# Kernel tuning notes

Measured on AMD Instinct MI355X. Metric: run time of the kernel, lower is better.

The kernel has to match this reference:

```python
import jax, jax.numpy as jnp
import numpy as np

B, M, N, P, H = 8192, 4, 2, 2, 128
D5 = M * 5            # FC5 output = m * in_mult_KNet
D2H = (H + H) * 40    # FC2 hidden = d_input_FC2 * out_mult_KNet


def _lin(x, W, b):
    return x @ W.T + b


def _gru(x, h, Wih, Whh, bih, bhh):
    # PyTorch GRU cell math (single layer, single step)
    gi = x @ Wih.T + bih   # [B, 3H]
    gh = h @ Whh.T + bhh   # [B, 3H]
    ir, iz, inn = jnp.split(gi, 3, axis=-1)
    hr, hz, hn = jnp.split(gh, 3, axis=-1)
    r = jax.nn.sigmoid(ir + hr)
    z = jax.nn.sigmoid(iz + hz)
    n = jnp.tanh(inn + r * hn)
    return (1.0 - z) * n + z * h


def setup_inputs() -> dict:
    key = jax.random.key(0)
    ks = iter(jax.random.split(key, 64))
    rn = lambda *s: jax.random.normal(next(ks), s, dtype=jnp.float32)
    sc = lambda d: np.float32(1.0 / np.sqrt(d))
    inp = {
        'y': rn(B, N, 1), 'u': rn(B, P, 1), 'm1x_post': rn(B, M, 1),
        'h_Q': jnp.zeros((B, H), jnp.float32),
        'h_Sigma': jnp.zeros((B, H), jnp.float32),
        'h_S': jnp.zeros((B, H), jnp.float32),
        'F_mat': jnp.eye(M, dtype=jnp.float32) + 0.1 * rn(M, M),
        'G_mat': 0.1 * rn(M, P),
        'H_mat': 0.5 * rn(N, M),
        'innov_logit': jnp.float32(0.0),
        'W_fc5': rn(D5, M) * sc(M), 'b_fc5': rn(D5) * 0.01,
        'Wih_Q': rn(3 * H, D5) * sc(H), 'Whh_Q': rn(3 * H, H) * sc(H),
        'bih_Q': rn(3 * H) * 0.01, 'bhh_Q': rn(3 * H) * 0.01,
        'Wih_Sig': rn(3 * H, H) * sc(H), 'Whh_Sig': rn(3 * H, H) * sc(H),
        'bih_Sig': rn(3 * H) * 0.01, 'bhh_Sig': rn(3 * H) * 0.01,
        'W_fc1': rn(N * N, H) * sc(H), 'b_fc1': rn(N * N) * 0.01,
        'W_fc7': rn(N, N) * sc(N), 'b_fc7': rn(N) * 0.01,
        'Wih_S': rn(3 * H, N * N + N) * sc(H), 'Whh_S': rn(3 * H, H) * sc(H),
        'bih_S': rn(3 * H) * 0.01, 'bhh_S': rn(3 * H) * 0.01,
        'W_fc2a': rn(D2H, 2 * H) * sc(2 * H), 'b_fc2a': rn(D2H) * 0.01,
        'W_fc2b': rn(N * M, D2H) * sc(D2H), 'b_fc2b': rn(N * M) * 0.01,
        'W_fc3': rn(M * M, H + N * M) * sc(H + N * M), 'b_fc3': rn(M * M) * 0.01,
        'W_fc4': rn(H, H + M * M) * sc(H + M * M), 'b_fc4': rn(H) * 0.01,
    }
    return inp


def reference(y, u, m1x_post, h_Q, h_Sigma, h_S, F_mat, G_mat, H_mat, innov_logit,
              W_fc5, b_fc5, Wih_Q, Whh_Q, bih_Q, bhh_Q,
              Wih_Sig, Whh_Sig, bih_Sig, bhh_Sig,
              W_fc1, b_fc1, W_fc7, b_fc7,
              Wih_S, Whh_S, bih_S, bhh_S,
              W_fc2a, b_fc2a, W_fc2b, b_fc2b,
              W_fc3, b_fc3, W_fc4, b_fc4):
    relu = jax.nn.relu
    # --- step_prior: linear system model f(x,u)=Fx+Gu, h(x)=Hx (no normalization) ---
    x_post = m1x_post[..., 0]                      # [B, M]
    x_prior = x_post @ F_mat.T + u[..., 0] @ G_mat.T
    y_pred = x_prior @ H_mat.T                     # [B, N]
    dy = y[..., 0] - y_pred                        # innovation [B, N]
    # --- KGain_step (dropout = identity at inference) ---
    out5 = relu(_lin(x_prior, W_fc5, b_fc5))       # [B, 20]
    hQ_new = _gru(out5, h_Q, Wih_Q, Whh_Q, bih_Q, bhh_Q)
    hSig = _gru(hQ_new, h_Sigma, Wih_Sig, Whh_Sig, bih_Sig, bhh_Sig)
    out1 = relu(_lin(hSig, W_fc1, b_fc1))          # [B, n^2]
    out7 = relu(_lin(dy, W_fc7, b_fc7))            # [B, n]
    hS_new = _gru(jnp.concatenate([out1, out7], -1), h_S, Wih_S, Whh_S, bih_S, bhh_S)
    in2 = jnp.concatenate([hSig, hS_new], -1)      # [B, 256]
    out2 = _lin(relu(_lin(in2, W_fc2a, b_fc2a)), W_fc2b, b_fc2b)  # KG flat [B, n*m]
    out3 = relu(_lin(jnp.concatenate([hS_new, out2], -1), W_fc3, b_fc3))
    hSig_new = relu(_lin(jnp.concatenate([hSig, out3], -1), W_fc4, b_fc4))
    # --- posterior update ---
    KG = out2.reshape(B, M, N)
    gamma = jax.nn.sigmoid(innov_logit)
    inov = gamma * jnp.einsum('bmn,bn->bm', KG, dy)
    m1x_posterior = (x_prior + inov)[..., None]    # [B, M, 1]
    return m1x_posterior, hQ_new, hSig_new, hS_new
```

## Files before the change

kernel.cpp:

```cpp
#include <hip/hip_runtime.h>
#include <hip/hip_bf16.h>

typedef __attribute__((ext_vector_type(8))) short bf16x8;
typedef __attribute__((ext_vector_type(4))) float f32x4;
typedef __attribute__((ext_vector_type(4))) short s16x4;
typedef __attribute__((ext_vector_type(4))) float f32v4;
typedef unsigned short u16;

__device__ inline u16 f2b(float f){ __hip_bfloat16 b = __float2bfloat16(f); return __builtin_bit_cast(unsigned short, b); }
__device__ inline float b2f(u16 u){ unsigned int x = ((unsigned int)u)<<16; return __builtin_bit_cast(float, x); }
__device__ inline float sigm(float x){ return 1.f/(1.f+__expf(-x)); }
__device__ inline float tanhfast(float x){ float e = __expf(2.f*x); return 1.f - 2.f/(e+1.f); }

__device__ inline f32x4 mfma16(bf16x8 a, bf16x8 b, f32x4 c){
  return __builtin_amdgcn_mfma_f32_16x16x32_bf16(a, b, c, 0, 0, 0);
}

struct CVA {
  const float *w2a, *w2b, *wihQ, *whhQ, *wihSg, *whhSg, *wihS, *whhS, *wfc3, *wfc4;
  u16 *waB, *wbB, *wihQp, *whhQb, *wihSgB, *whhSgB, *wihSp, *whhSb, *wfc3p, *wfc4p;
};

__global__ __launch_bounds__(256) void kconv(CVA a){
  int id = blockIdx.x*256 + threadIdx.x;
  if (id < 2621440){
    int t  = id >> 12;
    int r  = id & 4095;
    int kk = r >> 9;
    int l  = (r >> 3) & 63;
    int e  = id & 7;
    int col = t*16 + (l & 15);
    int k   = kk*32 + (l >> 4)*8 + e;
    a.waB[id] = f2b(a.w2a[col*256 + k]);
    return;
  }
  id -= 2621440;
  if (id < 163840){
    int s = id >> 9;
    int r = id & 511;
    int l = r >> 3;
    int e = r & 7;
    int o = l & 15;
    int k = s*32 + (l >> 4)*8 + e;
    a.wbB[id] = (o < 8) ? f2b(a.w2b[o*10240 + k]) : (u16)0;
    return;
  }
  id -= 163840;
  if (id < 12288){ int j=id>>5, k=id&31; a.wihQp[id] = (k<20)? f2b(a.wihQ[j*20+k]) : (u16)0; return; }
  id -= 12288;
  if (id < 49152){ a.whhQb[id] = f2b(a.whhQ[id]); return; }
  id -= 49152;
  if (id < 49152){ a.wihSgB[id] = f2b(a.wihSg[id]); return; }
  id -= 49152;
  if (id < 49152){ a.whhSgB[id] = f2b(a.whhSg[id]); return; }
  id -= 49152;
  if (id < 12288){ int j=id>>5, k=id&31; a.wihSp[id] = (k<6)? f2b(a.wihS[j*6+k]) : (u16)0; return; }
  id -= 12288;
  if (id < 49152){ a.whhSb[id] = f2b(a.whhS[id]); return; }
  id -= 49152;
  if (id < 2560){ int j=id/160, k=id%160; a.wfc3p[id] = (k<136)? f2b(a.wfc3[j*136+k]) : (u16)0; return; }
  id -= 2560;
  if (id < 20480){ int j=id/160, k=id%160; a.wfc4p[id] = (k<144)? f2b(a.wfc4[j*144+k]) : (u16)0; return; }
}

template<int KX, int LDX, bool SOUT, bool GB16, bool GF32>
__device__ __forceinline__ void gru_step(
    const u16* sX, const u16* sH,
    const u16* __restrict__ Wih, const int ldwih, const u16* __restrict__ Whh,
    const float* __restrict__ bih, const float* __restrict__ bhh,
    float* __restrict__ gOutF, u16* sOut, u16* __restrict__ gB16)
{
  const int tid = threadIdx.x;
  const int w = tid>>6, lane = tid&63, c = lane&15, khi = lane>>4;
  for (int nn=0; nn<2; ++nn){
    const int n = w*2+nn;
    const int j = n*16 + c;
    const float bir=bih[j], biz=bih[128+j], bin=bih[256+j];
    const float bhr=bhh[j], bhz=bhh[128+j], bhn=bhh[256+j];
    bf16x8 BX0[KX], BX1[KX], BX2[KX], BH0[4], BH1[4], BH2[4];
    #pragma unroll
    for (int kk=0;kk<KX;++kk){
      const u16* p = Wih + j*ldwih + kk*32 + khi*8;
      BX0[kk] = *(const bf16x8*)(p);
      BX1[kk] = *(const bf16x8*)(p + 128*ldwih);
      BX2[kk] = *(const bf16x8*)(p + 256*ldwih);
    }
    #pragma unroll
    for (int kk=0;kk<4;++kk){
      const u16* p = Whh + j*128 + kk*32 + khi*8;
      BH0[kk] = *(const bf16x8*)(p);
      BH1[kk] = *(const bf16x8*)(p + 128*128);
      BH2[kk] = *(const bf16x8*)(p + 256*128);
    }
    #pragma unroll
    for (int m=0;m<2;++m){
      f32x4 ir={0,0,0,0}, iz={0,0,0,0}, inx={0,0,0,0};
      f32x4 hr={0,0,0,0}, hz={0,0,0,0}, hn={0,0,0,0};
      #pragma unroll
      for (int kk=0;kk<KX;++kk){
        bf16x8 A = *(const bf16x8*)(sX + (m*16+c)*LDX + kk*32 + khi*8);
        ir  = mfma16(A, BX0[kk], ir);
        iz  = mfma16(A, BX1[kk], iz);
        inx = mfma16(A, BX2[kk], inx);
      }
      #pragma unroll
      for (int kk=0;kk<4;++kk){
        bf16x8 A = *(const bf16x8*)(sH + (m*16+c)*136 + kk*32 + khi*8);
        hr = mfma16(A, BH0[kk], hr);
        hz = mfma16(A, BH1[kk], hz);
        hn = mfma16(A, BH2[kk], hn);
      }
      #pragma unroll
      for (int e=0;e<4;++e){
        int r = m*16 + khi*4 + e;
        float rg = sigm(ir[e]+hr[e]+bir+bhr);
        float zg = sigm(iz[e]+hz[e]+biz+bhz);
        float ng = tanhfast(inx[e]+bin + rg*(hn[e]+bhn));
        float hold = b2f(sH[r*136 + j]);
        float hv = (1.f-zg)*ng + zg*hold;
        if (GF32) gOutF[r*128 + j] = hv;
        if (SOUT) sOut[r*136 + j] = f2b(hv);
        if (GB16) gB16[r*256 + j] = f2b(hv);
      }
    }
  }
}

struct K1A {
  const float *y,*u,*m1x,*hQ,*hSg,*hS,*F,*G,*Hm,*W5,*b5,
              *bihQ,*bhhQ,*bihSg,*bhhSg,*W1,*b1,*W7,*b7,*bihS,*bhhS;
  const u16 *wihQp,*whhQ,*wihSg,*whhSg,*wihSp,*whhS;
  float *outHQ,*outHS,*xp,*dy;
  u16 *in2;
};

__device__ __forceinline__ void load_h_tile(u16* dst, const float* src, int row0){
  const int tid = threadIdx.x;
  #pragma unroll
  for (int i=0;i<4;++i){
    int f4 = tid + i*256;
    int r = f4>>5, c4 = f4&31;
    f32v4 v = *(const f32v4*)(src + (row0+r)*128 + c4*4);
    s16x4 o;
    o[0]=(short)f2b(v[0]); o[1]=(short)f2b(v[1]);
    o[2]=(short)f2b(v[2]); o[3]=(short)f2b(v[3]);
    *(s16x4*)(dst + r*136 + c4*4) = o;
  }
}

__global__ __launch_bounds__(256) void k1(K1A a){
  __shared__ u16 sX[32*40];
  __shared__ u16 sH[32*136];
  __shared__ u16 sXL[32*136];
  __shared__ u16 sSig[32*136];
  __shared__ float sDY[64];
  const int row0 = blockIdx.x*32;
  const int tid = threadIdx.x;

  load_h_tile(sH, a.hQ, row0);
  if (tid < 32){
    int r = tid, row = row0 + r;
    float xpost[4], uu[2], xpr[4];
    #pragma unroll
    for (int i=0;i<4;++i) xpost[i]=a.m1x[row*4+i];
    uu[0]=a.u[row*2]; uu[1]=a.u[row*2+1];
    #pragma unroll
    for (int i=0;i<4;++i){
      float s=0.f;
      #pragma unroll
      for (int jj=0;jj<4;++jj) s += a.F[i*4+jj]*xpost[jj];
      #pragma unroll
      for (int jj=0;jj<2;++jj) s += a.G[i*2+jj]*uu[jj];
      xpr[i]=s; a.xp[row*4+i]=s;
    }
    #pragma unroll
    for (int nn2=0;nn2<2;++nn2){
      float s=0.f;
      #pragma unroll
      for (int jj=0;jj<4;++jj) s += a.Hm[nn2*4+jj]*xpr[jj];
      float d = a.y[row*2+nn2]-s;
      a.dy[row*2+nn2]=d; sDY[r*2+nn2]=d;
    }
    #pragma unroll
    for (int o=0;o<20;++o){
      float s=a.b5[o];
      #pragma unroll
      for (int k=0;k<4;++k) s += a.W5[o*4+k]*xpr[k];
      sX[r*40+o]=f2b(fmaxf(s,0.f));
    }
    for (int o=20;o<40;++o) sX[r*40+o]=0;
  }
  __syncthreads();
  gru_step<1,40,true,false,true>(sX, sH, a.wihQp, 32, a.whhQ, a.bihQ, a.bhhQ,
                                 a.outHQ + row0*128, sXL, nullptr);
  __syncthreads();
  load_h_tile(sH, a.hSg, row0);
  __syncthreads();
  gru_step<4,136,true,true,false>(sXL, sH, a.wihSg, 128, a.whhSg, a.bihSg, a.bhhSg,
                                  nullptr, sSig, a.in2 + row0*256);
  __syncthreads();
  if (tid < 128){
    int r = tid>>2, o = tid&3;
    float s = a.b1[o];
    for (int k=0;k<128;++k) s += a.W1[o*128+k]*b2f(sSig[r*136+k]);
    sX[r*40+o] = f2b(fmaxf(s,0.f));
  } else if (tid < 192){
    int t = tid-128; int r=t>>1, o=t&1;
    float s = a.b7[o] + a.W7[o*2]*sDY[r*2] + a.W7[o*2+1]*sDY[r*2+1];
    sX[r*40+4+o] = f2b(fmaxf(s,0.f));
  }
  for (int i=tid;i<32*26;i+=256){ int r=i/26, cc=6+(i%26); sX[r*40+cc]=0; }
  load_h_tile(sH, a.hS, row0);
  __syncthreads();
  gru_step<1,40,false,true,true>(sX, sH, a.wihSp, 32, a.whhS, a.bihS, a.bhhS,
                                 a.outHS + row0*128, nullptr, a.in2 + row0*256 + 128);
}

struct K2A {
  const u16 *waB, *wbB, *in2;
  const float *b2a;
  float *parts;
};

__global__ __launch_bounds__(512) void k2(K2A a){
  __shared__ u16 sA[64*256];
  __shared__ u16 sHid[8*64*36];
  const int bid = blockIdx.x;
  const int rb = bid>>3, ch = bid&7;
  const int row0 = rb*64;
  const int tid = threadIdx.x;
  const int wid = tid>>6, lane = tid&63, c = lane&15, khi = lane>>4;

  #pragma unroll
  for (int i=0;i<8;++i){
    int idx = tid + i*512;
    int r = idx>>6, c4 = idx&63;
    s16x4 v = *(const s16x4*)(a.in2 + (size_t)(row0+r)*256 + c4*4);
    *(s16x4*)(sA + r*256 + ((c4*4) ^ ((r&7)<<3))) = v;
  }
  __syncthreads();

  u16* sHw = sHid + wid*2304;
  f32x4 C2[4];
  #pragma unroll
  for (int m=0;m<4;++m) C2[m] = (f32x4){0,0,0,0};

  for (int it=0; it<5; ++it){
    const int colb = ch*1280 + it*256 + wid*32;
    const int t0 = colb>>4;
    #pragma unroll
    for (int h=0;h<2;++h){
      bf16x8 Bf[8];
      #pragma unroll
      for (int kk=0;kk<8;++kk)
        Bf[kk] = *(const bf16x8*)(a.waB + (size_t)((t0+h)*8+kk)*512 + lane*8);
      const float bias = a.b2a[colb + h*16 + c];
      #pragma unroll
      for (int m=0;m<4;++m){
        const int row = m*16 + c;
        bf16x8 Af[8];
        #pragma unroll
        for (int kk=0;kk<8;++kk)
          Af[kk] = *(const bf16x8*)(sA + row*256 + ((kk*32 + khi*8) ^ ((row&7)<<3)));
        f32x4 c0={0,0,0,0};
        #pragma unroll
        for (int kk=0;kk<8;++kk)
          c0 = mfma16(Af[kk], Bf[kk], c0);
        #pragma unroll
        for (int e=0;e<4;++e){
          int rr = m*16 + khi*4 + e;
          sHw[rr*36 + h*16 + c] = f2b(fmaxf(c0[e]+bias, 0.f));
        }
      }
    }
    bf16x8 B2 = *(const bf16x8*)(a.wbB + (size_t)(colb>>5)*512 + lane*8);
    #pragma unroll
    for (int m=0;m<4;++m){
      bf16x8 A2 = *(const bf16x8*)(sHw + (m*16+c)*36 + khi*8);
      C2[m] = mfma16(A2, B2, C2[m]);
    }
  }
  __syncthreads();
  float* sRed = (float*)sHid;
  if (c < 8){
    #pragma unroll
    for (int m=0;m<4;++m)
      #pragma unroll
      for (int e=0;e<4;++e)
        sRed[wid*512 + (m*16+khi*4+e)*8 + c] = C2[m][e];
  }
  __syncthreads();
  {
    int i = tid;
    int r = i>>3, o = i&7;
    float s = 0.f;
    #pragma unroll
    for (int wv=0;wv<8;++wv) s += sRed[wv*512 + r*8 + o];
    a.parts[(size_t)ch*65536 + (size_t)(row0+r)*8 + o] = s;
  }
}

struct K3A {
  const float *parts;
  const float *b2b, *bfc3, *bfc4, *xp, *dy, *innov;
  const u16 *in2, *wfc3p, *wfc4p;
  float *outPost, *outHSig;
};

__global__ __launch_bounds__(256) void k3(K3A a){
  __shared__ u16 sA[64*168];
  __shared__ u16 sX4[64*168];
  __shared__ float sOut2[64*8];
  const int row0 = blockIdx.x*64;
  const int tid = threadIdx.x;
  for (int i=tid;i<512;i+=256){
    int r=i>>3, o=i&7, row=row0+r;
    float s = a.b2b[o];
    #pragma unroll
    for (int chv=0;chv<8;++chv) s += a.parts[chv*65536 + row*8 + o];
    sOut2[i]=s;
    sA[r*168+128+o]=f2b(s);
  }
  for (int i=tid;i<2048;i+=256){
    int r=i>>5, c4=i&31;
    *(s16x4*)(sA  + r*168 + c4*4) = *(const s16x4*)(a.in2 + (row0+r)*256 + 128 + c4*4);
    *(s16x4*)(sX4 + r*168 + c4*4) = *(const s16x4*)(a.in2 + (row0+r)*256 + c4*4);
  }
  for (int i=tid;i<64*6;i+=256){
    int r=i/6, c4=i%6;
    *(s16x4*)(sA + r*168 + 136 + c4*4) = (s16x4){0,0,0,0};
  }
  for (int i=tid;i<64*4;i+=256){
    int r=i>>2, c4=i&3;
    *(s16x4*)(sX4 + r*168 + 144 + c4*4) = (s16x4){0,0,0,0};
  }
  __syncthreads();
  {
    int r = tid>>2, m = tid&3, row = row0+r;
    float g = 1.f/(1.f+__expf(-a.innov[0]));
    float d0 = a.dy[row*2], d1 = a.dy[row*2+1];
    float k0 = sOut2[r*8+m*2], k1 = sOut2[r*8+m*2+1];
    a.outPost[row*4+m] = a.xp[row*4+m] + g*(k0*d0+k1*d1);
  }
  const int w = tid>>6, lane = tid&63, c = lane&15, khi = lane>>4;
  {
    f32x4 C3 = {0,0,0,0};
    #pragma unroll
    for (int kk=0;kk<5;++kk){
      bf16x8 A  = *(const bf16x8*)(sA + (w*16+c)*168 + kk*32 + khi*8);
      bf16x8 Bf = *(const bf16x8*)(a.wfc3p + c*160 + kk*32 + khi*8);
      C3 = mfma16(A,Bf,C3);
    }
    float bj = a.bfc3[c];
    #pragma unroll
    for (int e=0;e<4;++e){
      int r = w*16 + khi*4 + e;
      sX4[r*168 + 128 + c] = f2b(fmaxf(C3[e]+bj, 0.f));
    }
  }
  __syncthreads();
  for (int nn=0;nn<2;++nn){
    int j = (w*2+nn)*16 + c;
    bf16x8 Bf[5];
    #pragma unroll
    for (int kk=0;kk<5;++kk) Bf[kk] = *(const bf16x8*)(a.wfc4p + j*160 + kk*32 + khi*8);
    float bj = a.bfc4[j];
    #pragma unroll
    for (int m=0;m<4;++m){
      f32x4 C = {0,0,0,0};
      #pragma unroll
      for (int kk=0;kk<5;++kk){
        bf16x8 A = *(const bf16x8*)(sX4 + (m*16+c)*168 + kk*32 + khi*8);
        C = mfma16(A, Bf[kk], C);
      }
      #pragma unroll
      for (int e=0;e<4;++e){
        int r = m*16 + khi*4 + e;
        a.outHSig[(row0+r)*128 + j] = fmaxf(C[e]+bj, 0.f);
      }
    }
  }
}

extern "C" void kernel_launch(void* const* d_in, const int* in_sizes, int n_in,
                              void* d_out, int out_size, void* d_ws, size_t ws_size,
                              hipStream_t stream){
  const float* y    = (const float*)d_in[0];
  const float* u    = (const float*)d_in[1];
  const float* m1x  = (const float*)d_in[2];
  const float* hQ   = (const float*)d_in[3];
  const float* hSg  = (const float*)d_in[4];
  const float* hS   = (const float*)d_in[5];
  const float* F    = (const float*)d_in[6];
  const float* G    = (const float*)d_in[7];
  const float* Hm   = (const float*)d_in[8];
  const float* innov= (const float*)d_in[9];
  const float* W5   = (const float*)d_in[10];
  const float* b5   = (const float*)d_in[11];
  const float* WihQ = (const float*)d_in[12];
  const float* WhhQ = (const float*)d_in[13];
  const float* bihQ = (const float*)d_in[14];
  const float* bhhQ = (const float*)d_in[15];
  const float* WihSg= (const float*)d_in[16];
  const float* WhhSg= (const float*)d_in[17];
  const float* bihSg= (const float*)d_in[18];
  const float* bhhSg= (const float*)d_in[19];
  const float* W1   = (const float*)d_in[20];
  const float* b1   = (const float*)d_in[21];
  const float* W7   = (const float*)d_in[22];
  const float* b7   = (const float*)d_in[23];
  const float* WihS = (const float*)d_in[24];
  const float* WhhS = (const float*)d_in[25];
  const float* bihS = (const float*)d_in[26];
  const float* bhhS = (const float*)d_in[27];
  const float* W2a  = (const float*)d_in[28];
  const float* b2a  = (const float*)d_in[29];
  const float* W2b  = (const float*)d_in[30];
  const float* b2b  = (const float*)d_in[31];
  const float* W3   = (const float*)d_in[32];
  const float* b3   = (const float*)d_in[33];
  const float* W4   = (const float*)d_in[34];
  const float* b4   = (const float*)d_in[35];

  const size_t WS_NEEDED = 12547072;
  if (ws_size < WS_NEEDED) return;

  char* ws = (char*)d_ws;
  u16*  waB   = (u16*)(ws + 0);
  u16*  wbB   = (u16*)(ws + 5242880);
  u16*  in2B  = (u16*)(ws + 5570560);
  float* parts= (float*)(ws + 9764864);
  float* xp   = (float*)(ws + 11862016);
  float* dyb  = (float*)(ws + 11993088);
  u16* wihQp  = (u16*)(ws + 12058624);
  u16* whhQb  = (u16*)(ws + 12083200);
  u16* wihSgB = (u16*)(ws + 12181504);
  u16* whhSgB = (u16*)(ws + 12279808);
  u16* wihSp  = (u16*)(ws + 12378112);
  u16* whhSb  = (u16*)(ws + 12402688);
  u16* wfc3p  = (u16*)(ws + 12500992);
  u16* wfc4p  = (u16*)(ws + 12506112);

  float* outF    = (float*)d_out;
  float* outPost = outF;
  float* outHQ   = outF + 32768;
  float* outHSig = outF + 32768 + 1048576;
  float* outHS   = outF + 32768 + 2*1048576;

  CVA cv{W2a, W2b, WihQ, WhhQ, WihSg, WhhSg, WihS, WhhS, W3, W4,
         waB, wbB, wihQp, whhQb, wihSgB, whhSgB, wihSp, whhSb, wfc3p, wfc4p};
  kconv<<<dim3(11834), dim3(256), 0, stream>>>(cv);

  K1A a1{y,u,m1x,hQ,hSg,hS,F,G,Hm,W5,b5,bihQ,bhhQ,bihSg,bhhSg,W1,b1,W7,b7,bihS,bhhS,
         wihQp,whhQb,wihSgB,whhSgB,wihSp,whhSb,
         outHQ,outHS,xp,dyb,in2B};
  k1<<<dim3(256), dim3(256), 0, stream>>>(a1);

  K2A a2{waB, wbB, in2B, b2a, parts};
  k2<<<dim3(1024), dim3(512), 0, stream>>>(a2);

  K3A a3{parts, b2b, b3, b4, xp, dyb, innov, in2B, wfc3p, wfc4p, outPost, outHSig};
  k3<<<dim3(128), dim3(256), 0, stream>>>(a3);
}
```

Baseline: 104.5 us.

## Use 32x32 MFMA and 128-row tiles in the FC2 kernel

Reworks the large FC2a/FC2b GEMM kernel to use 32x32x16 bf16 MFMA instructions instead of 16x16x32, with the weight pre-layout in the conversion kernel changed to match. Each block now covers 128 rows instead of 64 and the grid is halved, so every streamed weight fragment is reused across twice as many rows. The aim is to cut global weight traffic and instruction count per FLOP. In exchange the shared-memory footprint per block and the accumulator register pressure both grow, which may reduce occupancy.

```diff
diff --git a/kernel.cpp b/kernel.cpp
--- a/kernel.cpp
+++ b/kernel.cpp
@@ -3,6 +3,7 @@
 
 typedef __attribute__((ext_vector_type(8))) short bf16x8;
 typedef __attribute__((ext_vector_type(4))) float f32x4;
+typedef __attribute__((ext_vector_type(16))) float f32x16;
 typedef __attribute__((ext_vector_type(4))) short s16x4;
 typedef __attribute__((ext_vector_type(4))) float f32v4;
 typedef unsigned short u16;
@@ -15,6 +16,9 @@
 __device__ inline f32x4 mfma16(bf16x8 a, bf16x8 b, f32x4 c){
   return __builtin_amdgcn_mfma_f32_16x16x32_bf16(a, b, c, 0, 0, 0);
 }
+__device__ inline f32x16 mfma32(bf16x8 a, bf16x8 b, f32x16 c){
+  return __builtin_amdgcn_mfma_f32_32x32x16_bf16(a, b, c, 0, 0, 0);
+}
 
 struct CVA {
   const float *w2a, *w2b, *wihQ, *whhQ, *wihSg, *whhSg, *wihS, *whhS, *wfc3, *wfc4;
@@ -24,13 +28,13 @@
 __global__ __launch_bounds__(256) void kconv(CVA a){
   int id = blockIdx.x*256 + threadIdx.x;
   if (id < 2621440){
-    int t  = id >> 12;
-    int r  = id & 4095;
-    int kk = r >> 9;
-    int l  = (r >> 3) & 63;
-    int e  = id & 7;
-    int col = t*16 + (l & 15);
-    int k   = kk*32 + (l >> 4)*8 + e;
+    int t32 = id >> 13;
+    int rem = id & 8191;
+    int kk  = rem >> 9;
+    int l   = (rem >> 3) & 63;
+    int e   = id & 7;
+    int col = t32*32 + (l & 31);
+    int k   = kk*16 + (l >> 5)*8 + e;
     a.waB[id] = f2b(a.w2a[col*256 + k]);
     return;
   }
@@ -222,17 +226,19 @@
   float *parts;
 };
 
-__global__ __launch_bounds__(512) void k2(K2A a){
-  __shared__ u16 sA[64*256];
-  __shared__ u16 sHid[8*64*36];
+__global__ __launch_bounds__(512, 4) void k2(K2A a){
+  __shared__ u16 sA[128*256];
+  __shared__ u16 sHw[8][16*40];
   const int bid = blockIdx.x;
-  const int rb = bid>>3, ch = bid&7;
-  const int row0 = rb*64;
+  const int rg = bid>>3, ch = bid&7;
+  const int row0 = rg*128;
   const int tid = threadIdx.x;
-  const int wid = tid>>6, lane = tid&63, c = lane&15, khi = lane>>4;
+  const int wid = tid>>6, lane = tid&63;
+  const int c = lane&15, khi = lane>>4;
+  const int c32 = lane&31, hi = lane>>5;
 
   #pragma unroll
-  for (int i=0;i<8;++i){
+  for (int i=0;i<16;++i){
     int idx = tid + i*512;
     int r = idx>>6, c4 = idx&63;
     s16x4 v = *(const s16x4*)(a.in2 + (size_t)(row0+r)*256 + c4*4);
@@ -240,62 +246,59 @@
   }
   __syncthreads();
 
-  u16* sHw = sHid + wid*2304;
-  f32x4 C2[4];
+  f32x4 C2[8];
   #pragma unroll
-  for (int m=0;m<4;++m) C2[m] = (f32x4){0,0,0,0};
+  for (int m=0;m<8;++m) C2[m] = (f32x4){0,0,0,0};
 
   for (int it=0; it<5; ++it){
     const int colb = ch*1280 + it*256 + wid*32;
-    const int t0 = colb>>4;
-    #pragma unroll
-    for (int h=0;h<2;++h){
-      bf16x8 Bf[8];
-      #pragma unroll
-      for (int kk=0;kk<8;++kk)
-        Bf[kk] = *(const bf16x8*)(a.waB + (size_t)((t0+h)*8+kk)*512 + lane*8);
-      const float bias = a.b2a[colb + h*16 + c];
+    f32x16 C1[4];
+    #pragma unroll
+    for (int m=0;m<4;++m) C1[m] = (f32x16)(0.f);
+    const u16* waT = a.waB + (size_t)(colb>>5)*8192;
+    #pragma unroll
+    for (int kk=0;kk<16;++kk){
+      bf16x8 Bf = *(const bf16x8*)(waT + kk*512 + lane*8);
       #pragma unroll
       for (int m=0;m<4;++m){
-        const int row = m*16 + c;
-        bf16x8 Af[8];
+        const int row = m*32 + c32;
+        bf16x8 Af = *(const bf16x8*)(sA + row*256 + ((kk*16 + hi*8) ^ ((row&7)<<3)));
+        C1[m] = mfma32(Af, Bf, C1[m]);
+      }
+    }
+    const float bias = a.b2a[colb + c32];
+    bf16x8 B2 = *(const bf16x8*)(a.wbB + (size_t)(colb>>5)*512 + lane*8);
+    #pragma unroll
+    for (int m=0;m<4;++m){
+      #pragma unroll
+      for (int g=0; g<2; ++g){
         #pragma unroll
-        for (int kk=0;kk<8;++kk)
-          Af[kk] = *(const bf16x8*)(sA + row*256 + ((kk*32 + khi*8) ^ ((row&7)<<3)));
-        f32x4 c0={0,0,0,0};
-        #pragma unroll
-        for (int kk=0;kk<8;++kk)
-          c0 = mfma16(Af[kk], Bf[kk], c0);
-        #pragma unroll
-        for (int e=0;e<4;++e){
-          int rr = m*16 + khi*4 + e;
-          sHw[rr*36 + h*16 + c] = f2b(fmaxf(c0[e]+bias, 0.f));
+        for (int rr=0; rr<8; ++rr){
+          const int r16 = g*8 + rr;
+          const int rowl = (r16&3) + 8*((r16>>2)&1) + 4*hi;
+          sHw[wid][rowl*40 + c32] = f2b(fmaxf(C1[m][r16] + bias, 0.f));
         }
-      }
-    }
-    bf16x8 B2 = *(const bf16x8*)(a.wbB + (size_t)(colb>>5)*512 + lane*8);
-    #pragma unroll
-    for (int m=0;m<4;++m){
-      bf16x8 A2 = *(const bf16x8*)(sHw + (m*16+c)*36 + khi*8);
-      C2[m] = mfma16(A2, B2, C2[m]);
-    }
-  }
-  __syncthreads();
-  float* sRed = (float*)sHid;
+        bf16x8 A2 = *(const bf16x8*)(&sHw[wid][c*40 + khi*8]);
+        C2[m*2+g] = mfma16(A2, B2, C2[m*2+g]);
+      }
+    }
+  }
+  __syncthreads();
+  float* sRed = (float*)sA;
   if (c < 8){
     #pragma unroll
-    for (int m=0;m<4;++m)
+    for (int m=0;m<8;++m)
       #pragma unroll
       for (int e=0;e<4;++e)
-        sRed[wid*512 + (m*16+khi*4+e)*8 + c] = C2[m][e];
-  }
-  __syncthreads();
-  {
-    int i = tid;
-    int r = i>>3, o = i&7;
-    float s = 0.f;
-    #pragma unroll
-    for (int wv=0;wv<8;++wv) s += sRed[wv*512 + r*8 + o];
+        sRed[wid*1024 + (m*16 + khi*4 + e)*8 + c] = C2[m][e];
+  }
+  __syncthreads();
+  #pragma unroll
+  for (int i=tid; i<1024; i+=512){
+    int r=i>>3, o=i&7;
+    float s=0.f;
+    #pragma unroll
+    for (int wv=0; wv<8; ++wv) s += sRed[wv*1024 + r*8 + o];
     a.parts[(size_t)ch*65536 + (size_t)(row0+r)*8 + o] = s;
   }
 }
@@ -457,7 +460,7 @@
   k1<<<dim3(256), dim3(256), 0, stream>>>(a1);
 
   K2A a2{waB, wbB, in2B, b2a, parts};
-  k2<<<dim3(1024), dim3(512), 0, stream>>>(a2);
+  k2<<<dim3(512), dim3(512), 0, stream>>>(a2);
 
   K3A a3{parts, b2b, b3, b4, xp, dyb, innov, in2B, wfc3p, wfc4p, outPost, outHSig};
   k3<<<dim3(128), dim3(256), 0, stream>>>(a3);
```

Result: slower. 320.5 us (+206.6%).
